# Kernel tuning notes

Measured on AMD Instinct MI355X. Metric: run time of the kernel, lower is better.

## Reference

```python
import jax, jax.numpy as jnp
import numpy as np

N_NODES = 50000


def mean_aggregate(x, src, dst):
    # gather source features, scatter-sum to destinations, divide by in-degree
    msgs = x[src]                                             # [E, D]
    summed = jax.ops.segment_sum(msgs, dst, num_segments=N_NODES)  # [N, D]
    deg = jax.ops.segment_sum(jnp.ones_like(dst, dtype=x.dtype), dst,
                              num_segments=N_NODES)           # [N]
    return summed / jnp.clip(deg, 1.0)[:, None]


def sage_conv(x, src, dst, Wl, Wr, b):
    # PyG SAGEConv (aggr='mean'): lin_l(agg) + lin_r(x); bias only on lin_l
    agg = mean_aggregate(x, src, dst)
    return agg @ Wl + b + x @ Wr


def setup_inputs() -> dict:
    key = jax.random.key(0)
    ks = jax.random.split(key, 8)
    x = jax.random.normal(ks[0], (N_NODES, 64), dtype=jnp.float32)
    edge_index = jax.random.randint(ks[1], (2, 800000), 0, N_NODES, dtype=jnp.int32)
    W1l = jax.random.normal(ks[2], (64, 128), dtype=jnp.float32) * (1.0 / np.sqrt(64))
    W1r = jax.random.normal(ks[3], (64, 128), dtype=jnp.float32) * (1.0 / np.sqrt(64))
    b1 = jnp.zeros((128,), dtype=jnp.float32)
    W2l = jax.random.normal(ks[4], (128, 40), dtype=jnp.float32) * (1.0 / np.sqrt(128))
    W2r = jax.random.normal(ks[5], (128, 40), dtype=jnp.float32) * (1.0 / np.sqrt(128))
    b2 = jnp.zeros((40,), dtype=jnp.float32)
    return {"x": x, "edge_index": edge_index, "W1l": W1l, "W1r": W1r, "b1": b1,
            "W2l": W2l, "W2r": W2r, "b2": b2}


def reference(x, edge_index, W1l, W1r, b1, W2l, W2r, b2):
    src, dst = edge_index[0], edge_index[1]
    h = sage_conv(x, src, dst, W1l, W1r, b1)
    h = jax.nn.relu(h)
    # dropout p=0.5 is identity in eval mode (self.training=False)
    h = sage_conv(h, src, dst, W2l, W2r, b2)
    return h, jax.nn.log_softmax(h, axis=1)
```

## Files before the change

### kernel.cpp

```cpp
#include <hip/hip_runtime.h>
#include <hip/hip_bf16.h>
#include <math.h>

#define N_NODES 50000
#define N_EDGES 800000
#define D0 64
#define D1 128
#define D2 40
#define SLOTS 64

typedef short s16x8 __attribute__((ext_vector_type(8)));
typedef float f32x4 __attribute__((ext_vector_type(4)));

static __device__ __forceinline__ unsigned short f2bf(float v) {
    __hip_bfloat16 hb = __float2bfloat16(v);
    return *(unsigned short*)&hb;
}

__global__ __launch_bounds__(256) void prep_scatter_kernel(
        const float* __restrict__ x, const int* __restrict__ src, const int* __restrict__ dst,
        const float* __restrict__ W1l, const float* __restrict__ W1r,
        const float* __restrict__ W2l, const float* __restrict__ W2r,
        unsigned short* __restrict__ xh, int* __restrict__ deg, int* __restrict__ csr,
        unsigned short* __restrict__ wpk1, unsigned short* __restrict__ wpk2,
        int E, int nScat, int nCast) {
    int b = blockIdx.x, t = threadIdx.x;
    if (b < nScat) {
        int e0 = b * 2048;
#pragma unroll
        for (int i = t; i < 2048; i += 256) {
            int e = e0 + i;
            if (e < E) {
                int d = dst[e];
                int s = src[e];
                int slot = atomicAdd(&deg[d], 1);
                if (slot < SLOTS) csr[((size_t)d << 6) + slot] = s;
            }
        }
    } else if (b < nScat + nCast) {
        int i = ((b - nScat) * 256 + t) * 4;
        float4 v = *(const float4*)(x + i);
        unsigned o0 = (unsigned)f2bf(v.x) | ((unsigned)f2bf(v.y) << 16);
        unsigned o1 = (unsigned)f2bf(v.z) | ((unsigned)f2bf(v.w) << 16);
        uint2 pk; pk.x = o0; pk.y = o1;
        *(uint2*)(xh + i) = pk;
    } else if (b < nScat + nCast + 8) {
        int f = (b - nScat - nCast) * 4 + (t >> 6);
        int lane = t & 63;
        int nt = f & 7;
        int col = nt * 16 + (lane & 15);
        int kbase = (f >> 3) * 32 + (lane >> 4) * 8;
        unsigned short* o = wpk1 + ((size_t)f * 64 + lane) * 8;
#pragma unroll
        for (int j = 0; j < 8; ++j) {
            int k = kbase + j;
            float w = (k < 64) ? W1r[k * 128 + col] : W1l[(k - 64) * 128 + col];
            o[j] = f2bf(w);
        }
    } else {
        int f = (b - nScat - nCast - 8) * 4 + (t >> 6);
        if (f < 20) {
            int lane = t & 63;
            int nt = f % 5;
            int col = nt * 16 + (lane & 15);
            int kbase = (f / 5) * 32 + (lane >> 4) * 8;
            unsigned short* o = wpk2 + ((size_t)f * 64 + lane) * 8;
#pragma unroll
            for (int j = 0; j < 8; ++j) {
                int k = kbase + j;
                float w = (col < 40) ? W2l[k * 40 + col] : W2r[k * 40 + (col - 40)];
                o[j] = f2bf(w);
            }
        }
    }
}


__global__ void agg1_kernel(const unsigned short* __restrict__ xh,
                            const int* __restrict__ rowcnt,
                            const int* __restrict__ csr, unsigned short* __restrict__ aggh, int N) {
    int wid = (blockIdx.x * blockDim.x + threadIdx.x) >> 6;
    int lane = threadIdx.x & 63;
    if (wid >= N) return;
    int beg = wid << 6;
    int deg = rowcnt[wid];
    int l = lane & 7, g = lane >> 3;
    float acc[8];
#pragma unroll
    for (int k = 0; k < 8; ++k) acc[k] = 0.f;
    int jmax = (deg + 7) >> 3;
    int full = jmax - 1;
    int j = 0;
    for (; j + 2 <= full; j += 2) {
        int s0 = csr[beg + j * 8 + g];
        int s1 = csr[beg + (j + 1) * 8 + g];
        uint4 v0 = *(const uint4*)(xh + (size_t)s0 * D0 + l * 8);
        uint4 v1 = *(const uint4*)(xh + (size_t)s1 * D0 + l * 8);
        acc[0] += __uint_as_float(v0.x << 16);          acc[1] += __uint_as_float(v0.x & 0xffff0000u);
        acc[2] += __uint_as_float(v0.y << 16);          acc[3] += __uint_as_float(v0.y & 0xffff0000u);
        acc[4] += __uint_as_float(v0.z << 16);          acc[5] += __uint_as_float(v0.z & 0xffff0000u);
        acc[6] += __uint_as_float(v0.w << 16);          acc[7] += __uint_as_float(v0.w & 0xffff0000u);
        acc[0] += __uint_as_float(v1.x << 16);          acc[1] += __uint_as_float(v1.x & 0xffff0000u);
        acc[2] += __uint_as_float(v1.y << 16);          acc[3] += __uint_as_float(v1.y & 0xffff0000u);
        acc[4] += __uint_as_float(v1.z << 16);          acc[5] += __uint_as_float(v1.z & 0xffff0000u);
        acc[6] += __uint_as_float(v1.w << 16);          acc[7] += __uint_as_float(v1.w & 0xffff0000u);
    }
    if (j < full) {
        int s0 = csr[beg + j * 8 + g];
        uint4 v0 = *(const uint4*)(xh + (size_t)s0 * D0 + l * 8);
        acc[0] += __uint_as_float(v0.x << 16);          acc[1] += __uint_as_float(v0.x & 0xffff0000u);
        acc[2] += __uint_as_float(v0.y << 16);          acc[3] += __uint_as_float(v0.y & 0xffff0000u);
        acc[4] += __uint_as_float(v0.z << 16);          acc[5] += __uint_as_float(v0.z & 0xffff0000u);
        acc[6] += __uint_as_float(v0.w << 16);          acc[7] += __uint_as_float(v0.w & 0xffff0000u);
    }
    if (jmax > 0) {
        int slot = full * 8 + g;
        int e = beg + ((slot < deg) ? slot : (deg - 1));
        int s0 = csr[e];
        float w = (slot < deg) ? 1.f : 0.f;
        uint4 v0 = *(const uint4*)(xh + (size_t)s0 * D0 + l * 8);
        acc[0] = fmaf(w, __uint_as_float(v0.x << 16), acc[0]);
        acc[1] = fmaf(w, __uint_as_float(v0.x & 0xffff0000u), acc[1]);
        acc[2] = fmaf(w, __uint_as_float(v0.y << 16), acc[2]);
        acc[3] = fmaf(w, __uint_as_float(v0.y & 0xffff0000u), acc[3]);
        acc[4] = fmaf(w, __uint_as_float(v0.z << 16), acc[4]);
        acc[5] = fmaf(w, __uint_as_float(v0.z & 0xffff0000u), acc[5]);
        acc[6] = fmaf(w, __uint_as_float(v0.w << 16), acc[6]);
        acc[7] = fmaf(w, __uint_as_float(v0.w & 0xffff0000u), acc[7]);
    }
#pragma unroll
    for (int off = 8; off <= 32; off <<= 1) {
#pragma unroll
        for (int k = 0; k < 8; ++k) acc[k] += __shfl_xor(acc[k], off);
    }
    float inv = 1.f / (float)max(deg, 1);
    if (g == 0) {
        unsigned o0 = (unsigned)f2bf(acc[0] * inv) | ((unsigned)f2bf(acc[1] * inv) << 16);
        unsigned o1 = (unsigned)f2bf(acc[2] * inv) | ((unsigned)f2bf(acc[3] * inv) << 16);
        unsigned o2 = (unsigned)f2bf(acc[4] * inv) | ((unsigned)f2bf(acc[5] * inv) << 16);
        unsigned o3 = (unsigned)f2bf(acc[6] * inv) | ((unsigned)f2bf(acc[7] * inv) << 16);
        uint4 pk; pk.x = o0; pk.y = o1; pk.z = o2; pk.w = o3;
        *(uint4*)(aggh + (size_t)wid * D0 + l * 8) = pk;
    }
}


__global__ void agg2_kernel(const unsigned short* __restrict__ p2h, const float* __restrict__ r2,
                            const int* __restrict__ rowcnt,
                            const int* __restrict__ csr,
                            float* __restrict__ out, float* __restrict__ out2, int N) {
    int wid = (blockIdx.x * blockDim.x + threadIdx.x) >> 6;
    int lane = threadIdx.x & 63;
    if (wid >= N) return;
    int beg = wid << 6;
    int deg = rowcnt[wid];
    int g = lane / 5;
    int l = lane - g * 5;
    bool gv = g < 12;
    float a[8];
#pragma unroll
    for (int k = 0; k < 8; ++k) a[k] = 0.f;
    int jmax = (deg + 11) / 12;
    int full = jmax - 1;
    int j = 0;
    for (; j + 2 <= full; j += 2) {
        int s0 = csr[beg + j * 12 + g];
        int s1 = csr[beg + (j + 1) * 12 + g];
        uint4 v0 = *(const uint4*)(p2h + (size_t)s0 * 64 + l * 8);
        uint4 v1 = *(const uint4*)(p2h + (size_t)s1 * 64 + l * 8);
        if (gv) {
            a[0] += __uint_as_float(v0.x << 16);  a[1] += __uint_as_float(v0.x & 0xffff0000u);
            a[2] += __uint_as_float(v0.y << 16);  a[3] += __uint_as_float(v0.y & 0xffff0000u);
            a[4] += __uint_as_float(v0.z << 16);  a[5] += __uint_as_float(v0.z & 0xffff0000u);
            a[6] += __uint_as_float(v0.w << 16);  a[7] += __uint_as_float(v0.w & 0xffff0000u);
            a[0] += __uint_as_float(v1.x << 16);  a[1] += __uint_as_float(v1.x & 0xffff0000u);
            a[2] += __uint_as_float(v1.y << 16);  a[3] += __uint_as_float(v1.y & 0xffff0000u);
            a[4] += __uint_as_float(v1.z << 16);  a[5] += __uint_as_float(v1.z & 0xffff0000u);
            a[6] += __uint_as_float(v1.w << 16);  a[7] += __uint_as_float(v1.w & 0xffff0000u);
        }
    }
    if (j < full) {
        int s0 = csr[beg + j * 12 + g];
        uint4 v0 = *(const uint4*)(p2h + (size_t)s0 * 64 + l * 8);
        if (gv) {
            a[0] += __uint_as_float(v0.x << 16);  a[1] += __uint_as_float(v0.x & 0xffff0000u);
            a[2] += __uint_as_float(v0.y << 16);  a[3] += __uint_as_float(v0.y & 0xffff0000u);
            a[4] += __uint_as_float(v0.z << 16);  a[5] += __uint_as_float(v0.z & 0xffff0000u);
            a[6] += __uint_as_float(v0.w << 16);  a[7] += __uint_as_float(v0.w & 0xffff0000u);
        }
    }
    if (jmax > 0) {
        int slot = full * 12 + g;
        int e = beg + ((slot < deg) ? slot : (deg - 1));
        int s0 = csr[e];
        float w = (gv && slot < deg) ? 1.f : 0.f;
        uint4 v0 = *(const uint4*)(p2h + (size_t)s0 * 64 + l * 8);
        a[0] = fmaf(w, __uint_as_float(v0.x << 16), a[0]);
        a[1] = fmaf(w, __uint_as_float(v0.x & 0xffff0000u), a[1]);
        a[2] = fmaf(w, __uint_as_float(v0.y << 16), a[2]);
        a[3] = fmaf(w, __uint_as_float(v0.y & 0xffff0000u), a[3]);
        a[4] = fmaf(w, __uint_as_float(v0.z << 16), a[4]);
        a[5] = fmaf(w, __uint_as_float(v0.z & 0xffff0000u), a[5]);
        a[6] = fmaf(w, __uint_as_float(v0.w << 16), a[6]);
        a[7] = fmaf(w, __uint_as_float(v0.w & 0xffff0000u), a[7]);
    }
    {
        float b0;
#pragma unroll
        for (int k = 0; k < 8; ++k) { b0 = __shfl(a[k], lane + 30); if (g < 6) a[k] += b0; }
#pragma unroll
        for (int k = 0; k < 8; ++k) { b0 = __shfl(a[k], lane + 15); if (g < 3) a[k] += b0; }
#pragma unroll
        for (int k = 0; k < 8; ++k) {
            float b1 = __shfl(a[k], lane + 5);
            float b2 = __shfl(a[k], lane + 10);
            if (g == 0) a[k] += b1 + b2;
        }
    }
    float inv = 1.f / (float)max(deg, 1);
    bool wr = (lane < 5);
    float h2[8];
    if (wr) {
        float4 ra = *(const float4*)(r2 + (size_t)wid * D2 + lane * 8);
        float4 rb = *(const float4*)(r2 + (size_t)wid * D2 + lane * 8 + 4);
        h2[0] = ra.x + a[0] * inv; h2[1] = ra.y + a[1] * inv;
        h2[2] = ra.z + a[2] * inv; h2[3] = ra.w + a[3] * inv;
        h2[4] = rb.x + a[4] * inv; h2[5] = rb.y + a[5] * inv;
        h2[6] = rb.z + a[6] * inv; h2[7] = rb.w + a[7] * inv;
        float4 oa; oa.x = h2[0]; oa.y = h2[1]; oa.z = h2[2]; oa.w = h2[3];
        float4 ob; ob.x = h2[4]; ob.y = h2[5]; ob.z = h2[6]; ob.w = h2[7];
        *(float4*)(out + (size_t)wid * D2 + lane * 8) = oa;
        *(float4*)(out + (size_t)wid * D2 + lane * 8 + 4) = ob;
    }
    float m = -INFINITY;
    if (wr) {
#pragma unroll
        for (int k = 0; k < 8; ++k) m = fmaxf(m, h2[k]);
    }
#pragma unroll
    for (int off = 1; off < 64; off <<= 1) m = fmaxf(m, __shfl_xor(m, off));
    float s = 0.f;
    if (wr) {
#pragma unroll
        for (int k = 0; k < 8; ++k) s += expf(h2[k] - m);
    }
#pragma unroll
    for (int off = 1; off < 64; off <<= 1) s += __shfl_xor(s, off);
    if (wr) {
        float lg = m + logf(s);
        float4 oa; oa.x = h2[0] - lg; oa.y = h2[1] - lg; oa.z = h2[2] - lg; oa.w = h2[3] - lg;
        float4 ob; ob.x = h2[4] - lg; ob.y = h2[5] - lg; ob.z = h2[6] - lg; ob.w = h2[7] - lg;
        *(float4*)(out2 + (size_t)wid * D2 + lane * 8) = oa;
        *(float4*)(out2 + (size_t)wid * D2 + lane * 8 + 4) = ob;
    }
}

__global__ __launch_bounds__(256) void gemm_fused(
        const unsigned short* __restrict__ xh, const unsigned short* __restrict__ aggh,
        const unsigned short* __restrict__ Wpk1, const unsigned short* __restrict__ Wpk2,
        const float* __restrict__ b1, const float* __restrict__ b2,
        unsigned short* __restrict__ p2h, float* __restrict__ r2, int N) {
    __shared__ __align__(16) unsigned short As[64 * 136];
    int t = threadIdx.x;
    int r0 = blockIdx.x * 64;
    for (int i = t; i < 1024; i += 256) {
        int r = i >> 4, c = i & 15;
        int gr = r0 + r; gr = (gr < N) ? gr : (N - 1);
        uint4 v = (c < 8) ? ((const uint4*)(xh + (size_t)gr * 64))[c]
                          : ((const uint4*)(aggh + (size_t)gr * 64))[c - 8];
        *(uint4*)(As + r * 136 + c * 8) = v;
    }
    __syncthreads();
    int w = t >> 6, lane = t & 63;
    int l15 = lane & 15, q = lane >> 4;
    f32x4 zero = {0.f, 0.f, 0.f, 0.f};
    const unsigned short* abase = As + (w * 16 + l15) * 136 + q * 8;

    f32x4 acc[8];
#pragma unroll
    for (int nt = 0; nt < 8; ++nt) acc[nt] = zero;
#pragma unroll
    for (int ks = 0; ks < 4; ++ks) {
        s16x8 a0 = *(const s16x8*)(abase + ks * 32);
        s16x8 b[8];
#pragma unroll
        for (int nt = 0; nt < 8; ++nt)
            b[nt] = *(const s16x8*)(Wpk1 + ((size_t)(ks * 8 + nt) * 64 + lane) * 8);
#pragma unroll
        for (int nt = 0; nt < 8; ++nt)
            acc[nt] = __builtin_amdgcn_mfma_f32_16x16x32_bf16(a0, b[nt], acc[nt], 0, 0, 0);
    }
    int rloc = w * 16 + q * 4;
#pragma unroll
    for (int nt = 0; nt < 8; ++nt) {
        int col = nt * 16 + l15;
        float bias = b1[col];
#pragma unroll
        for (int reg = 0; reg < 4; ++reg)
            As[(rloc + reg) * 136 + col] = f2bf(fmaxf(acc[nt][reg] + bias, 0.f));
    }
    f32x4 acc2[5];
#pragma unroll
    for (int nt = 0; nt < 5; ++nt) acc2[nt] = zero;
#pragma unroll
    for (int ks = 0; ks < 4; ++ks) {
        s16x8 a0 = *(const s16x8*)(abase + ks * 32);
        s16x8 b[5];
#pragma unroll
        for (int nt = 0; nt < 5; ++nt)
            b[nt] = *(const s16x8*)(Wpk2 + ((size_t)(ks * 5 + nt) * 64 + lane) * 8);
#pragma unroll
        for (int nt = 0; nt < 5; ++nt)
            acc2[nt] = __builtin_amdgcn_mfma_f32_16x16x32_bf16(a0, b[nt], acc2[nt], 0, 0, 0);
    }
    int rbase = r0 + w * 16 + q * 4;
#pragma unroll
    for (int nt = 0; nt < 5; ++nt) {
        int col = nt * 16 + l15;
        bool isp = col < 40;
        int oc = isp ? col : (col - 40);
        float bias = isp ? 0.f : b2[oc];
#pragma unroll
        for (int reg = 0; reg < 4; ++reg) {
            int row = rbase + reg;
            if (row < N) {
                float v = acc2[nt][reg] + bias;
                if (isp) p2h[(size_t)row * 64 + oc] = f2bf(v);
                else     r2[(size_t)row * D2 + oc] = v;
            }
        }
    }
}


extern "C" void kernel_launch(void* const* d_in, const int* in_sizes, int n_in,
                              void* d_out, int out_size, void* d_ws, size_t ws_size,
                              hipStream_t stream) {
    const float* x   = (const float*)d_in[0];
    const int*   ei  = (const int*)d_in[1];
    const float* W1l = (const float*)d_in[2];
    const float* W1r = (const float*)d_in[3];
    const float* b1  = (const float*)d_in[4];
    const float* W2l = (const float*)d_in[5];
    const float* W2r = (const float*)d_in[6];
    const float* b2  = (const float*)d_in[7];
    float* out = (float*)d_out;

    const int N = N_NODES;
    const int E = in_sizes[1] / 2;
    const int* src = ei;
    const int* dst = ei + E;

    char* p = (char*)d_ws;
    auto alloc = [&](size_t bytes) -> void* {
        void* r = (void*)p;
        p += (bytes + 255) & ~(size_t)255;
        return r;
    };
    const int nScat = (E + 2047) / 2048;
    const int nCast = (N * D0) / 1024;

    int*      deg  = (int*)alloc((size_t)N * 4);
    int*      csr  = (int*)alloc((size_t)N * SLOTS * 4);
    unsigned short* xh    = (unsigned short*)alloc((size_t)N * D0 * 2);
    unsigned short* aggh  = (unsigned short*)alloc((size_t)N * D0 * 2);
    unsigned short* wpk1  = (unsigned short*)alloc((size_t)32 * 64 * 8 * 2);
    unsigned short* wpk2  = (unsigned short*)alloc((size_t)20 * 64 * 8 * 2);
    unsigned short* p2h   = (unsigned short*)alloc((size_t)N * 64 * 2);
    float* r2buf = (float*)alloc((size_t)N * D2 * 4);

    hipMemsetAsync(deg, 0, (size_t)N * sizeof(int), stream);
    prep_scatter_kernel<<<nScat + nCast + 8 + 5, 256, 0, stream>>>(
        x, src, dst, W1l, W1r, W2l, W2r, xh, deg, csr, wpk1, wpk2, E, nScat, nCast);

    agg1_kernel<<<(N * 64 + 255) / 256, 256, 0, stream>>>(xh, deg, csr, aggh, N);
    gemm_fused<<<(N + 63) / 64, 256, 0, stream>>>(xh, aggh, wpk1, wpk2, b1, b2,
                                                  p2h, r2buf, N);

    agg2_kernel<<<(N * 64 + 255) / 256, 256, 0, stream>>>(p2h, r2buf, deg, csr,
                                                          out, out + (size_t)N * D2, N);
}
```

Baseline: 192.9 us.

## Replace per-node CSR with destination buckets and shared-memory atomic aggregation

Edges are binned into 512 buckets of 98 destination nodes using block-local histograms and one global atomic per bucket, storing packed (local dst, src) words. Both aggregation kernels now process one bucket per block, accumulating features with LDS float atomics and computing degrees locally, replacing the padded 64-slot per-node CSR and the per-node global atomics. This reduces global atomic traffic and CSR memory, but it trades in lower block-level parallelism, heavy shared-memory atomics, and a serial per-thread log-softmax epilogue with strided stores. Buckets overflowing 2048 edges would silently drop edges.

```diff
diff --git a/kernel.cpp b/kernel.cpp
--- a/kernel.cpp
+++ b/kernel.cpp
@@ -7,7 +7,12 @@
 #define D0 64
 #define D1 128
 #define D2 40
-#define SLOTS 64
+
+#define NB  512
+#define NPB 98
+#define CAP 2048
+#define PAD1 68
+#define PAD2 41
 
 typedef short s16x8 __attribute__((ext_vector_type(8)));
 typedef float f32x4 __attribute__((ext_vector_type(4)));
@@ -21,20 +26,38 @@
         const float* __restrict__ x, const int* __restrict__ src, const int* __restrict__ dst,
         const float* __restrict__ W1l, const float* __restrict__ W1r,
         const float* __restrict__ W2l, const float* __restrict__ W2r,
-        unsigned short* __restrict__ xh, int* __restrict__ deg, int* __restrict__ csr,
+        unsigned short* __restrict__ xh, int* __restrict__ gcur, unsigned* __restrict__ ebuf,
         unsigned short* __restrict__ wpk1, unsigned short* __restrict__ wpk2,
         int E, int nScat, int nCast) {
     int b = blockIdx.x, t = threadIdx.x;
     if (b < nScat) {
-        int e0 = b * 2048;
-#pragma unroll
-        for (int i = t; i < 2048; i += 256) {
-            int e = e0 + i;
-            if (e < E) {
-                int d = dst[e];
-                int s = src[e];
-                int slot = atomicAdd(&deg[d], 1);
-                if (slot < SLOTS) csr[((size_t)d << 6) + slot] = s;
+        __shared__ int h[NB];
+        __shared__ int base[NB];
+        int e0 = b * 4096;
+        h[t] = 0; h[t + 256] = 0;
+        __syncthreads();
+        int dloc[16];
+#pragma unroll
+        for (int u = 0; u < 16; ++u) {
+            int e = e0 + u * 256 + t;
+            dloc[u] = (e < E) ? dst[e] : -1;
+            if (dloc[u] >= 0) atomicAdd(&h[(unsigned)dloc[u] / NPB], 1);
+        }
+        __syncthreads();
+        for (int u = t; u < NB; u += 256)
+            if (h[u] > 0) base[u] = u * CAP + atomicAdd(&gcur[u], h[u]);
+        __syncthreads();
+        h[t] = 0; h[t + 256] = 0;
+        __syncthreads();
+#pragma unroll
+        for (int u = 0; u < 16; ++u) {
+            int e = e0 + u * 256 + t;
+            if (dloc[u] >= 0) {
+                unsigned d = (unsigned)dloc[u];
+                unsigned bk = d / NPB;
+                unsigned ld = d - bk * NPB;
+                int k = atomicAdd(&h[bk], 1);
+                ebuf[base[bk] + k] = (ld << 17) | (unsigned)src[e];
             }
         }
     } else if (b < nScat + nCast) {
@@ -75,183 +98,124 @@
     }
 }
 
-
-__global__ void agg1_kernel(const unsigned short* __restrict__ xh,
-                            const int* __restrict__ rowcnt,
-                            const int* __restrict__ csr, unsigned short* __restrict__ aggh, int N) {
-    int wid = (blockIdx.x * blockDim.x + threadIdx.x) >> 6;
-    int lane = threadIdx.x & 63;
-    if (wid >= N) return;
-    int beg = wid << 6;
-    int deg = rowcnt[wid];
-    int l = lane & 7, g = lane >> 3;
-    float acc[8];
-#pragma unroll
-    for (int k = 0; k < 8; ++k) acc[k] = 0.f;
-    int jmax = (deg + 7) >> 3;
-    int full = jmax - 1;
-    int j = 0;
-    for (; j + 2 <= full; j += 2) {
-        int s0 = csr[beg + j * 8 + g];
-        int s1 = csr[beg + (j + 1) * 8 + g];
-        uint4 v0 = *(const uint4*)(xh + (size_t)s0 * D0 + l * 8);
-        uint4 v1 = *(const uint4*)(xh + (size_t)s1 * D0 + l * 8);
-        acc[0] += __uint_as_float(v0.x << 16);          acc[1] += __uint_as_float(v0.x & 0xffff0000u);
-        acc[2] += __uint_as_float(v0.y << 16);          acc[3] += __uint_as_float(v0.y & 0xffff0000u);
-        acc[4] += __uint_as_float(v0.z << 16);          acc[5] += __uint_as_float(v0.z & 0xffff0000u);
-        acc[6] += __uint_as_float(v0.w << 16);          acc[7] += __uint_as_float(v0.w & 0xffff0000u);
-        acc[0] += __uint_as_float(v1.x << 16);          acc[1] += __uint_as_float(v1.x & 0xffff0000u);
-        acc[2] += __uint_as_float(v1.y << 16);          acc[3] += __uint_as_float(v1.y & 0xffff0000u);
-        acc[4] += __uint_as_float(v1.z << 16);          acc[5] += __uint_as_float(v1.z & 0xffff0000u);
-        acc[6] += __uint_as_float(v1.w << 16);          acc[7] += __uint_as_float(v1.w & 0xffff0000u);
-    }
-    if (j < full) {
-        int s0 = csr[beg + j * 8 + g];
-        uint4 v0 = *(const uint4*)(xh + (size_t)s0 * D0 + l * 8);
-        acc[0] += __uint_as_float(v0.x << 16);          acc[1] += __uint_as_float(v0.x & 0xffff0000u);
-        acc[2] += __uint_as_float(v0.y << 16);          acc[3] += __uint_as_float(v0.y & 0xffff0000u);
-        acc[4] += __uint_as_float(v0.z << 16);          acc[5] += __uint_as_float(v0.z & 0xffff0000u);
-        acc[6] += __uint_as_float(v0.w << 16);          acc[7] += __uint_as_float(v0.w & 0xffff0000u);
-    }
-    if (jmax > 0) {
-        int slot = full * 8 + g;
-        int e = beg + ((slot < deg) ? slot : (deg - 1));
-        int s0 = csr[e];
-        float w = (slot < deg) ? 1.f : 0.f;
-        uint4 v0 = *(const uint4*)(xh + (size_t)s0 * D0 + l * 8);
-        acc[0] = fmaf(w, __uint_as_float(v0.x << 16), acc[0]);
-        acc[1] = fmaf(w, __uint_as_float(v0.x & 0xffff0000u), acc[1]);
-        acc[2] = fmaf(w, __uint_as_float(v0.y << 16), acc[2]);
-        acc[3] = fmaf(w, __uint_as_float(v0.y & 0xffff0000u), acc[3]);
-        acc[4] = fmaf(w, __uint_as_float(v0.z << 16), acc[4]);
-        acc[5] = fmaf(w, __uint_as_float(v0.z & 0xffff0000u), acc[5]);
-        acc[6] = fmaf(w, __uint_as_float(v0.w << 16), acc[6]);
-        acc[7] = fmaf(w, __uint_as_float(v0.w & 0xffff0000u), acc[7]);
-    }
-#pragma unroll
-    for (int off = 8; off <= 32; off <<= 1) {
-#pragma unroll
-        for (int k = 0; k < 8; ++k) acc[k] += __shfl_xor(acc[k], off);
-    }
-    float inv = 1.f / (float)max(deg, 1);
-    if (g == 0) {
-        unsigned o0 = (unsigned)f2bf(acc[0] * inv) | ((unsigned)f2bf(acc[1] * inv) << 16);
-        unsigned o1 = (unsigned)f2bf(acc[2] * inv) | ((unsigned)f2bf(acc[3] * inv) << 16);
-        unsigned o2 = (unsigned)f2bf(acc[4] * inv) | ((unsigned)f2bf(acc[5] * inv) << 16);
-        unsigned o3 = (unsigned)f2bf(acc[6] * inv) | ((unsigned)f2bf(acc[7] * inv) << 16);
+__global__ __launch_bounds__(256) void agg1_bucket(
+        const unsigned short* __restrict__ xh, const unsigned* __restrict__ ebuf,
+        const int* __restrict__ gcur, unsigned short* __restrict__ aggh, int N) {
+    __shared__ float acc[NPB][PAD1];
+    __shared__ int degL[NPB];
+    int b = blockIdx.x, t = threadIdx.x;
+    for (int i = t; i < NPB * PAD1; i += 256) ((float*)acc)[i] = 0.f;
+    if (t < NPB) degL[t] = 0;
+    __syncthreads();
+    int ne = gcur[b]; ne = (ne < CAP) ? ne : CAP;
+    const unsigned* eb = ebuf + (size_t)b * CAP;
+    int l = t & 7;
+    int g = t >> 3;
+    for (int i0 = 0; i0 < ne; i0 += 128) {
+        unsigned pk[4]; uint4 v[4]; bool val[4];
+#pragma unroll
+        for (int u = 0; u < 4; ++u) {
+            int e = i0 + u * 32 + g;
+            val[u] = e < ne;
+            pk[u] = eb[val[u] ? e : 0];
+            int sid = val[u] ? (int)(pk[u] & 0x1FFFFu) : 0;
+            v[u] = *(const uint4*)(xh + (size_t)sid * D0 + l * 8);
+        }
+#pragma unroll
+        for (int u = 0; u < 4; ++u) {
+            if (val[u]) {
+                int ld = (int)(pk[u] >> 17);
+                float* a = &acc[ld][l * 8];
+                atomicAdd(&a[0], __uint_as_float(v[u].x << 16));
+                atomicAdd(&a[1], __uint_as_float(v[u].x & 0xffff0000u));
+                atomicAdd(&a[2], __uint_as_float(v[u].y << 16));
+                atomicAdd(&a[3], __uint_as_float(v[u].y & 0xffff0000u));
+                atomicAdd(&a[4], __uint_as_float(v[u].z << 16));
+                atomicAdd(&a[5], __uint_as_float(v[u].z & 0xffff0000u));
+                atomicAdd(&a[6], __uint_as_float(v[u].w << 16));
+                atomicAdd(&a[7], __uint_as_float(v[u].w & 0xffff0000u));
+                if (l == 0) atomicAdd(&degL[ld], 1);
+            }
+        }
+    }
+    __syncthreads();
+    for (int i = t; i < NPB * 8; i += 256) {
+        int n = i >> 3, l8 = (i & 7) * 8;
+        int node = b * NPB + n;
+        if (node >= N) continue;
+        float inv = 1.f / (float)max(degL[n], 1);
+        const float* a = &acc[n][l8];
+        unsigned o0 = (unsigned)f2bf(a[0] * inv) | ((unsigned)f2bf(a[1] * inv) << 16);
+        unsigned o1 = (unsigned)f2bf(a[2] * inv) | ((unsigned)f2bf(a[3] * inv) << 16);
+        unsigned o2 = (unsigned)f2bf(a[4] * inv) | ((unsigned)f2bf(a[5] * inv) << 16);
+        unsigned o3 = (unsigned)f2bf(a[6] * inv) | ((unsigned)f2bf(a[7] * inv) << 16);
         uint4 pk; pk.x = o0; pk.y = o1; pk.z = o2; pk.w = o3;
-        *(uint4*)(aggh + (size_t)wid * D0 + l * 8) = pk;
-    }
-}
-
-
-__global__ void agg2_kernel(const unsigned short* __restrict__ p2h, const float* __restrict__ r2,
-                            const int* __restrict__ rowcnt,
-                            const int* __restrict__ csr,
-                            float* __restrict__ out, float* __restrict__ out2, int N) {
-    int wid = (blockIdx.x * blockDim.x + threadIdx.x) >> 6;
-    int lane = threadIdx.x & 63;
-    if (wid >= N) return;
-    int beg = wid << 6;
-    int deg = rowcnt[wid];
-    int g = lane / 5;
-    int l = lane - g * 5;
-    bool gv = g < 12;
-    float a[8];
-#pragma unroll
-    for (int k = 0; k < 8; ++k) a[k] = 0.f;
-    int jmax = (deg + 11) / 12;
-    int full = jmax - 1;
-    int j = 0;
-    for (; j + 2 <= full; j += 2) {
-        int s0 = csr[beg + j * 12 + g];
-        int s1 = csr[beg + (j + 1) * 12 + g];
-        uint4 v0 = *(const uint4*)(p2h + (size_t)s0 * 64 + l * 8);
-        uint4 v1 = *(const uint4*)(p2h + (size_t)s1 * 64 + l * 8);
-        if (gv) {
-            a[0] += __uint_as_float(v0.x << 16);  a[1] += __uint_as_float(v0.x & 0xffff0000u);
-            a[2] += __uint_as_float(v0.y << 16);  a[3] += __uint_as_float(v0.y & 0xffff0000u);
-            a[4] += __uint_as_float(v0.z << 16);  a[5] += __uint_as_float(v0.z & 0xffff0000u);
-            a[6] += __uint_as_float(v0.w << 16);  a[7] += __uint_as_float(v0.w & 0xffff0000u);
-            a[0] += __uint_as_float(v1.x << 16);  a[1] += __uint_as_float(v1.x & 0xffff0000u);
-            a[2] += __uint_as_float(v1.y << 16);  a[3] += __uint_as_float(v1.y & 0xffff0000u);
-            a[4] += __uint_as_float(v1.z << 16);  a[5] += __uint_as_float(v1.z & 0xffff0000u);
-            a[6] += __uint_as_float(v1.w << 16);  a[7] += __uint_as_float(v1.w & 0xffff0000u);
-        }
-    }
-    if (j < full) {
-        int s0 = csr[beg + j * 12 + g];
-        uint4 v0 = *(const uint4*)(p2h + (size_t)s0 * 64 + l * 8);
-        if (gv) {
-            a[0] += __uint_as_float(v0.x << 16);  a[1] += __uint_as_float(v0.x & 0xffff0000u);
-            a[2] += __uint_as_float(v0.y << 16);  a[3] += __uint_as_float(v0.y & 0xffff0000u);
-            a[4] += __uint_as_float(v0.z << 16);  a[5] += __uint_as_float(v0.z & 0xffff0000u);
-            a[6] += __uint_as_float(v0.w << 16);  a[7] += __uint_as_float(v0.w & 0xffff0000u);
-        }
-    }
-    if (jmax > 0) {
-        int slot = full * 12 + g;
-        int e = beg + ((slot < deg) ? slot : (deg - 1));
-        int s0 = csr[e];
-        float w = (gv && slot < deg) ? 1.f : 0.f;
-        uint4 v0 = *(const uint4*)(p2h + (size_t)s0 * 64 + l * 8);
-        a[0] = fmaf(w, __uint_as_float(v0.x << 16), a[0]);
-        a[1] = fmaf(w, __uint_as_float(v0.x & 0xffff0000u), a[1]);
-        a[2] = fmaf(w, __uint_as_float(v0.y << 16), a[2]);
-        a[3] = fmaf(w, __uint_as_float(v0.y & 0xffff0000u), a[3]);
-        a[4] = fmaf(w, __uint_as_float(v0.z << 16), a[4]);
-        a[5] = fmaf(w, __uint_as_float(v0.z & 0xffff0000u), a[5]);
-        a[6] = fmaf(w, __uint_as_float(v0.w << 16), a[6]);
-        a[7] = fmaf(w, __uint_as_float(v0.w & 0xffff0000u), a[7]);
-    }
-    {
-        float b0;
-#pragma unroll
-        for (int k = 0; k < 8; ++k) { b0 = __shfl(a[k], lane + 30); if (g < 6) a[k] += b0; }
-#pragma unroll
-        for (int k = 0; k < 8; ++k) { b0 = __shfl(a[k], lane + 15); if (g < 3) a[k] += b0; }
-#pragma unroll
-        for (int k = 0; k < 8; ++k) {
-            float b1 = __shfl(a[k], lane + 5);
-            float b2 = __shfl(a[k], lane + 10);
-            if (g == 0) a[k] += b1 + b2;
-        }
-    }
-    float inv = 1.f / (float)max(deg, 1);
-    bool wr = (lane < 5);
-    float h2[8];
-    if (wr) {
-        float4 ra = *(const float4*)(r2 + (size_t)wid * D2 + lane * 8);
-        float4 rb = *(const float4*)(r2 + (size_t)wid * D2 + lane * 8 + 4);
-        h2[0] = ra.x + a[0] * inv; h2[1] = ra.y + a[1] * inv;
-        h2[2] = ra.z + a[2] * inv; h2[3] = ra.w + a[3] * inv;
-        h2[4] = rb.x + a[4] * inv; h2[5] = rb.y + a[5] * inv;
-        h2[6] = rb.z + a[6] * inv; h2[7] = rb.w + a[7] * inv;
-        float4 oa; oa.x = h2[0]; oa.y = h2[1]; oa.z = h2[2]; oa.w = h2[3];
-        float4 ob; ob.x = h2[4]; ob.y = h2[5]; ob.z = h2[6]; ob.w = h2[7];
-        *(float4*)(out + (size_t)wid * D2 + lane * 8) = oa;
-        *(float4*)(out + (size_t)wid * D2 + lane * 8 + 4) = ob;
-    }
-    float m = -INFINITY;
-    if (wr) {
-#pragma unroll
-        for (int k = 0; k < 8; ++k) m = fmaxf(m, h2[k]);
-    }
-#pragma unroll
-    for (int off = 1; off < 64; off <<= 1) m = fmaxf(m, __shfl_xor(m, off));
-    float s = 0.f;
-    if (wr) {
-#pragma unroll
-        for (int k = 0; k < 8; ++k) s += expf(h2[k] - m);
-    }
-#pragma unroll
-    for (int off = 1; off < 64; off <<= 1) s += __shfl_xor(s, off);
-    if (wr) {
-        float lg = m + logf(s);
-        float4 oa; oa.x = h2[0] - lg; oa.y = h2[1] - lg; oa.z = h2[2] - lg; oa.w = h2[3] - lg;
-        float4 ob; ob.x = h2[4] - lg; ob.y = h2[5] - lg; ob.z = h2[6] - lg; ob.w = h2[7] - lg;
-        *(float4*)(out2 + (size_t)wid * D2 + lane * 8) = oa;
-        *(float4*)(out2 + (size_t)wid * D2 + lane * 8 + 4) = ob;
+        *(uint4*)(aggh + (size_t)node * D0 + l8) = pk;
+    }
+}
+
+__global__ __launch_bounds__(256) void agg2_bucket(
+        const unsigned short* __restrict__ p2h, const float* __restrict__ r2,
+        const unsigned* __restrict__ ebuf, const int* __restrict__ gcur,
+        float* __restrict__ out, float* __restrict__ out2, int N) {
+    __shared__ float acc[NPB][PAD2];
+    __shared__ int degL[NPB];
+    int b = blockIdx.x, t = threadIdx.x;
+    for (int i = t; i < NPB * PAD2; i += 256) ((float*)acc)[i] = 0.f;
+    if (t < NPB) degL[t] = 0;
+    __syncthreads();
+    int ne = gcur[b]; ne = (ne < CAP) ? ne : CAP;
+    const unsigned* eb = ebuf + (size_t)b * CAP;
+    int g = t / 5;
+    int l = t - g * 5;
+    bool gv = g < 51;
+    for (int i0 = 0; i0 < ne; i0 += 204) {
+        unsigned pk[4]; uint4 v[4]; bool val[4];
+#pragma unroll
+        for (int u = 0; u < 4; ++u) {
+            int e = i0 + u * 51 + g;
+            val[u] = gv && (e < ne);
+            pk[u] = eb[val[u] ? e : 0];
+            int sid = val[u] ? (int)(pk[u] & 0x1FFFFu) : 0;
+            v[u] = *(const uint4*)(p2h + (size_t)sid * 64 + l * 8);
+        }
+#pragma unroll
+        for (int u = 0; u < 4; ++u) {
+            if (val[u]) {
+                int ld = (int)(pk[u] >> 17);
+                float* a = &acc[ld][l * 8];
+                atomicAdd(&a[0], __uint_as_float(v[u].x << 16));
+                atomicAdd(&a[1], __uint_as_float(v[u].x & 0xffff0000u));
+                atomicAdd(&a[2], __uint_as_float(v[u].y << 16));
+                atomicAdd(&a[3], __uint_as_float(v[u].y & 0xffff0000u));
+                atomicAdd(&a[4], __uint_as_float(v[u].z << 16));
+                atomicAdd(&a[5], __uint_as_float(v[u].z & 0xffff0000u));
+                atomicAdd(&a[6], __uint_as_float(v[u].w << 16));
+                atomicAdd(&a[7], __uint_as_float(v[u].w & 0xffff0000u));
+                if (l == 0) atomicAdd(&degL[ld], 1);
+            }
+        }
+    }
+    __syncthreads();
+    if (t < NPB) {
+        int node = b * NPB + t;
+        if (node < N) {
+            float inv = 1.f / (float)max(degL[t], 1);
+            const float* rr = r2 + (size_t)node * D2;
+            float* ha = acc[t];
+            float m = -INFINITY;
+            for (int d = 0; d < D2; ++d) {
+                float h = rr[d] + ha[d] * inv;
+                ha[d] = h;
+                out[(size_t)node * D2 + d] = h;
+                m = fmaxf(m, h);
+            }
+            float s = 0.f;
+            for (int d = 0; d < D2; ++d) s += expf(ha[d] - m);
+            float lg = m + logf(s);
+            for (int d = 0; d < D2; ++d)
+                out2[(size_t)node * D2 + d] = ha[d] - lg;
+        }
     }
 }
 
@@ -357,11 +321,11 @@
         p += (bytes + 255) & ~(size_t)255;
         return r;
     };
-    const int nScat = (E + 2047) / 2048;
+    const int nScat = (E + 4095) / 4096;
     const int nCast = (N * D0) / 1024;
 
-    int*      deg  = (int*)alloc((size_t)N * 4);
-    int*      csr  = (int*)alloc((size_t)N * SLOTS * 4);
+    unsigned* ebuf = (unsigned*)alloc((size_t)NB * CAP * 4);
+    int*      gcur = (int*)alloc(NB * 4);
     unsigned short* xh    = (unsigned short*)alloc((size_t)N * D0 * 2);
     unsigned short* aggh  = (unsigned short*)alloc((size_t)N * D0 * 2);
     unsigned short* wpk1  = (unsigned short*)alloc((size_t)32 * 64 * 8 * 2);
@@ -369,14 +333,14 @@
     unsigned short* p2h   = (unsigned short*)alloc((size_t)N * 64 * 2);
     float* r2buf = (float*)alloc((size_t)N * D2 * 4);
 
-    hipMemsetAsync(deg, 0, (size_t)N * sizeof(int), stream);
+    hipMemsetAsync(gcur, 0, NB * sizeof(int), stream);
     prep_scatter_kernel<<<nScat + nCast + 8 + 5, 256, 0, stream>>>(
-        x, src, dst, W1l, W1r, W2l, W2r, xh, deg, csr, wpk1, wpk2, E, nScat, nCast);
-
-    agg1_kernel<<<(N * 64 + 255) / 256, 256, 0, stream>>>(xh, deg, csr, aggh, N);
+        x, src, dst, W1l, W1r, W2l, W2r, xh, gcur, ebuf, wpk1, wpk2, E, nScat, nCast);
+
+    agg1_bucket<<<NB, 256, 0, stream>>>(xh, ebuf, gcur, aggh, N);
     gemm_fused<<<(N + 63) / 64, 256, 0, stream>>>(xh, aggh, wpk1, wpk2, b1, b2,
                                                   p2h, r2buf, N);
 
-    agg2_kernel<<<(N * 64 + 255) / 256, 256, 0, stream>>>(p2h, r2buf, deg, csr,
-                                                          out, out + (size_t)N * D2, N);
-}
+    agg2_bucket<<<NB, 256, 0, stream>>>(p2h, r2buf, ebuf, gcur,
+                                        out, out + (size_t)N * D2, N);
+}
```

Result: slower. 555.5 us (+188.0%).

## Replace per-node slot CSR with bucketed two-pass edge sort and fused agg1

Applied to the files above, without the earlier changes.

Edge scattering changes from per-node global atomics into fixed 64-slot rows to a two-level bucket sort. Each block builds a shared-memory histogram of 49-node buckets, reserves space with one global atomic per bucket, and writes packed (local dst, src) words. A new fused kernel then builds a compact per-bucket CSR in LDS, emits rowstart/rowcnt for layer 2, and runs layer-1 aggregation directly from the LDS CSR. The aim is fewer contended global atomics and a smaller, denser CSR. The cost is a fixed per-bucket capacity of 1024 edges, which silently drops edges if a bucket overflows, and only 1024 blocks for the aggregation.

```diff
diff --git a/kernel.cpp b/kernel.cpp
--- a/kernel.cpp
+++ b/kernel.cpp
@@ -3,11 +3,13 @@
 #include <math.h>
 
 #define N_NODES 50000
-#define N_EDGES 800000
 #define D0 64
 #define D1 128
 #define D2 40
-#define SLOTS 64
+
+#define NB  1024
+#define NPB 49
+#define CAP 1024
 
 typedef short s16x8 __attribute__((ext_vector_type(8)));
 typedef float f32x4 __attribute__((ext_vector_type(4)));
@@ -21,20 +23,38 @@
         const float* __restrict__ x, const int* __restrict__ src, const int* __restrict__ dst,
         const float* __restrict__ W1l, const float* __restrict__ W1r,
         const float* __restrict__ W2l, const float* __restrict__ W2r,
-        unsigned short* __restrict__ xh, int* __restrict__ deg, int* __restrict__ csr,
+        unsigned short* __restrict__ xh, int* __restrict__ gcur, unsigned* __restrict__ ebuf,
         unsigned short* __restrict__ wpk1, unsigned short* __restrict__ wpk2,
         int E, int nScat, int nCast) {
     int b = blockIdx.x, t = threadIdx.x;
     if (b < nScat) {
-        int e0 = b * 2048;
-#pragma unroll
-        for (int i = t; i < 2048; i += 256) {
-            int e = e0 + i;
-            if (e < E) {
-                int d = dst[e];
-                int s = src[e];
-                int slot = atomicAdd(&deg[d], 1);
-                if (slot < SLOTS) csr[((size_t)d << 6) + slot] = s;
+        __shared__ int h[NB];
+        __shared__ int base[NB];
+        int e0 = b * 4096;
+        h[t] = 0; h[t + 256] = 0; h[t + 512] = 0; h[t + 768] = 0;
+        __syncthreads();
+        int dloc[16];
+#pragma unroll
+        for (int u = 0; u < 16; ++u) {
+            int e = e0 + u * 256 + t;
+            dloc[u] = (e < E) ? dst[e] : -1;
+            if (dloc[u] >= 0) atomicAdd(&h[(unsigned)dloc[u] / NPB], 1);
+        }
+        __syncthreads();
+        for (int u = t; u < NB; u += 256)
+            if (h[u] > 0) base[u] = u * CAP + atomicAdd(&gcur[u], h[u]);
+        __syncthreads();
+        h[t] = 0; h[t + 256] = 0; h[t + 512] = 0; h[t + 768] = 0;
+        __syncthreads();
+#pragma unroll
+        for (int u = 0; u < 16; ++u) {
+            int e = e0 + u * 256 + t;
+            if (dloc[u] >= 0) {
+                unsigned d = (unsigned)dloc[u];
+                unsigned bk = d / NPB;
+                unsigned ld = d - bk * NPB;
+                int k = atomicAdd(&h[bk], 1);
+                ebuf[base[bk] + k] = (ld << 17) | (unsigned)src[e];
             }
         }
     } else if (b < nScat + nCast) {
@@ -75,84 +95,139 @@
     }
 }
 
-
-__global__ void agg1_kernel(const unsigned short* __restrict__ xh,
-                            const int* __restrict__ rowcnt,
-                            const int* __restrict__ csr, unsigned short* __restrict__ aggh, int N) {
-    int wid = (blockIdx.x * blockDim.x + threadIdx.x) >> 6;
-    int lane = threadIdx.x & 63;
-    if (wid >= N) return;
-    int beg = wid << 6;
-    int deg = rowcnt[wid];
+__global__ __launch_bounds__(256) void fillagg1_kernel(
+        const unsigned short* __restrict__ xh, const unsigned* __restrict__ ebuf,
+        const int* __restrict__ gcur,
+        int* __restrict__ rowstart, int* __restrict__ rowcnt, int* __restrict__ csr,
+        unsigned short* __restrict__ aggh, int N) {
+    __shared__ int csr_l[CAP];
+    __shared__ int cnt[64];
+    __shared__ int sd[64];
+    __shared__ int rs[64];
+    __shared__ int pos[64];
+    int b = blockIdx.x, t = threadIdx.x;
+    int s0 = b * CAP;
+    int ne = gcur[b]; ne = (ne < CAP) ? ne : CAP;
+    unsigned ev[4];
+#pragma unroll
+    for (int u = 0; u < 4; ++u) {
+        int i = t + u * 256;
+        ev[u] = (i < ne) ? ebuf[s0 + i] : 0xFFFFFFFFu;
+    }
+    if (t < 64) cnt[t] = 0;
+    __syncthreads();
+#pragma unroll
+    for (int u = 0; u < 4; ++u)
+        if (ev[u] != 0xFFFFFFFFu) atomicAdd(&cnt[ev[u] >> 17], 1);
+    __syncthreads();
+    if (t < 64) sd[t] = cnt[t];
+    __syncthreads();
+    for (int off = 1; off < 64; off <<= 1) {
+        int u = (t >= off && t < 64) ? sd[t - off] : 0;
+        __syncthreads();
+        if (t < 64) sd[t] += u;
+        __syncthreads();
+    }
+    if (t < 64) {
+        int ex = sd[t] - cnt[t];
+        rs[t] = ex;
+        pos[t] = ex;
+    }
+    __syncthreads();
+#pragma unroll
+    for (int u = 0; u < 4; ++u) {
+        if (ev[u] != 0xFFFFFFFFu) {
+            int ld = (int)(ev[u] >> 17);
+            int p = atomicAdd(&pos[ld], 1);
+            csr_l[p] = (int)(ev[u] & 0x1FFFFu);
+        }
+    }
+    if (t < NPB) {
+        int node = b * NPB + t;
+        if (node < N) {
+            rowstart[node] = s0 + rs[t];
+            rowcnt[node] = cnt[t];
+        }
+    }
+    __syncthreads();
+    for (int i = t; i < ne; i += 256) csr[s0 + i] = csr_l[i];
+
+    int w = t >> 6, lane = t & 63;
     int l = lane & 7, g = lane >> 3;
-    float acc[8];
-#pragma unroll
-    for (int k = 0; k < 8; ++k) acc[k] = 0.f;
-    int jmax = (deg + 7) >> 3;
-    int full = jmax - 1;
-    int j = 0;
-    for (; j + 2 <= full; j += 2) {
-        int s0 = csr[beg + j * 8 + g];
-        int s1 = csr[beg + (j + 1) * 8 + g];
-        uint4 v0 = *(const uint4*)(xh + (size_t)s0 * D0 + l * 8);
-        uint4 v1 = *(const uint4*)(xh + (size_t)s1 * D0 + l * 8);
-        acc[0] += __uint_as_float(v0.x << 16);          acc[1] += __uint_as_float(v0.x & 0xffff0000u);
-        acc[2] += __uint_as_float(v0.y << 16);          acc[3] += __uint_as_float(v0.y & 0xffff0000u);
-        acc[4] += __uint_as_float(v0.z << 16);          acc[5] += __uint_as_float(v0.z & 0xffff0000u);
-        acc[6] += __uint_as_float(v0.w << 16);          acc[7] += __uint_as_float(v0.w & 0xffff0000u);
-        acc[0] += __uint_as_float(v1.x << 16);          acc[1] += __uint_as_float(v1.x & 0xffff0000u);
-        acc[2] += __uint_as_float(v1.y << 16);          acc[3] += __uint_as_float(v1.y & 0xffff0000u);
-        acc[4] += __uint_as_float(v1.z << 16);          acc[5] += __uint_as_float(v1.z & 0xffff0000u);
-        acc[6] += __uint_as_float(v1.w << 16);          acc[7] += __uint_as_float(v1.w & 0xffff0000u);
-    }
-    if (j < full) {
-        int s0 = csr[beg + j * 8 + g];
-        uint4 v0 = *(const uint4*)(xh + (size_t)s0 * D0 + l * 8);
-        acc[0] += __uint_as_float(v0.x << 16);          acc[1] += __uint_as_float(v0.x & 0xffff0000u);
-        acc[2] += __uint_as_float(v0.y << 16);          acc[3] += __uint_as_float(v0.y & 0xffff0000u);
-        acc[4] += __uint_as_float(v0.z << 16);          acc[5] += __uint_as_float(v0.z & 0xffff0000u);
-        acc[6] += __uint_as_float(v0.w << 16);          acc[7] += __uint_as_float(v0.w & 0xffff0000u);
-    }
-    if (jmax > 0) {
-        int slot = full * 8 + g;
-        int e = beg + ((slot < deg) ? slot : (deg - 1));
-        int s0 = csr[e];
-        float w = (slot < deg) ? 1.f : 0.f;
-        uint4 v0 = *(const uint4*)(xh + (size_t)s0 * D0 + l * 8);
-        acc[0] = fmaf(w, __uint_as_float(v0.x << 16), acc[0]);
-        acc[1] = fmaf(w, __uint_as_float(v0.x & 0xffff0000u), acc[1]);
-        acc[2] = fmaf(w, __uint_as_float(v0.y << 16), acc[2]);
-        acc[3] = fmaf(w, __uint_as_float(v0.y & 0xffff0000u), acc[3]);
-        acc[4] = fmaf(w, __uint_as_float(v0.z << 16), acc[4]);
-        acc[5] = fmaf(w, __uint_as_float(v0.z & 0xffff0000u), acc[5]);
-        acc[6] = fmaf(w, __uint_as_float(v0.w << 16), acc[6]);
-        acc[7] = fmaf(w, __uint_as_float(v0.w & 0xffff0000u), acc[7]);
-    }
-#pragma unroll
-    for (int off = 8; off <= 32; off <<= 1) {
-#pragma unroll
-        for (int k = 0; k < 8; ++k) acc[k] += __shfl_xor(acc[k], off);
-    }
-    float inv = 1.f / (float)max(deg, 1);
-    if (g == 0) {
-        unsigned o0 = (unsigned)f2bf(acc[0] * inv) | ((unsigned)f2bf(acc[1] * inv) << 16);
-        unsigned o1 = (unsigned)f2bf(acc[2] * inv) | ((unsigned)f2bf(acc[3] * inv) << 16);
-        unsigned o2 = (unsigned)f2bf(acc[4] * inv) | ((unsigned)f2bf(acc[5] * inv) << 16);
-        unsigned o3 = (unsigned)f2bf(acc[6] * inv) | ((unsigned)f2bf(acc[7] * inv) << 16);
-        uint4 pk; pk.x = o0; pk.y = o1; pk.z = o2; pk.w = o3;
-        *(uint4*)(aggh + (size_t)wid * D0 + l * 8) = pk;
+    for (int n = w; n < NPB; n += 4) {
+        int node = b * NPB + n;
+        if (node >= N) break;
+        int beg = rs[n];
+        int deg = cnt[n];
+        float acc[8];
+#pragma unroll
+        for (int k = 0; k < 8; ++k) acc[k] = 0.f;
+        int jmax = (deg + 7) >> 3;
+        int full = jmax - 1;
+        int j = 0;
+        for (; j + 2 <= full; j += 2) {
+            int s0e = csr_l[beg + j * 8 + g];
+            int s1e = csr_l[beg + (j + 1) * 8 + g];
+            uint4 v0 = *(const uint4*)(xh + (size_t)s0e * D0 + l * 8);
+            uint4 v1 = *(const uint4*)(xh + (size_t)s1e * D0 + l * 8);
+            acc[0] += __uint_as_float(v0.x << 16);  acc[1] += __uint_as_float(v0.x & 0xffff0000u);
+            acc[2] += __uint_as_float(v0.y << 16);  acc[3] += __uint_as_float(v0.y & 0xffff0000u);
+            acc[4] += __uint_as_float(v0.z << 16);  acc[5] += __uint_as_float(v0.z & 0xffff0000u);
+            acc[6] += __uint_as_float(v0.w << 16);  acc[7] += __uint_as_float(v0.w & 0xffff0000u);
+            acc[0] += __uint_as_float(v1.x << 16);  acc[1] += __uint_as_float(v1.x & 0xffff0000u);
+            acc[2] += __uint_as_float(v1.y << 16);  acc[3] += __uint_as_float(v1.y & 0xffff0000u);
+            acc[4] += __uint_as_float(v1.z << 16);  acc[5] += __uint_as_float(v1.z & 0xffff0000u);
+            acc[6] += __uint_as_float(v1.w << 16);  acc[7] += __uint_as_float(v1.w & 0xffff0000u);
+        }
+        if (j < full) {
+            int s0e = csr_l[beg + j * 8 + g];
+            uint4 v0 = *(const uint4*)(xh + (size_t)s0e * D0 + l * 8);
+            acc[0] += __uint_as_float(v0.x << 16);  acc[1] += __uint_as_float(v0.x & 0xffff0000u);
+            acc[2] += __uint_as_float(v0.y << 16);  acc[3] += __uint_as_float(v0.y & 0xffff0000u);
+            acc[4] += __uint_as_float(v0.z << 16);  acc[5] += __uint_as_float(v0.z & 0xffff0000u);
+            acc[6] += __uint_as_float(v0.w << 16);  acc[7] += __uint_as_float(v0.w & 0xffff0000u);
+        }
+        if (jmax > 0) {
+            int slot = full * 8 + g;
+            int e = beg + ((slot < deg) ? slot : (deg - 1));
+            int s0e = csr_l[e];
+            float wgt = (slot < deg) ? 1.f : 0.f;
+            uint4 v0 = *(const uint4*)(xh + (size_t)s0e * D0 + l * 8);
+            acc[0] = fmaf(wgt, __uint_as_float(v0.x << 16), acc[0]);
+            acc[1] = fmaf(wgt, __uint_as_float(v0.x & 0xffff0000u), acc[1]);
+            acc[2] = fmaf(wgt, __uint_as_float(v0.y << 16), acc[2]);
+            acc[3] = fmaf(wgt, __uint_as_float(v0.y & 0xffff0000u), acc[3]);
+            acc[4] = fmaf(wgt, __uint_as_float(v0.z << 16), acc[4]);
+            acc[5] = fmaf(wgt, __uint_as_float(v0.z & 0xffff0000u), acc[5]);
+            acc[6] = fmaf(wgt, __uint_as_float(v0.w << 16), acc[6]);
+            acc[7] = fmaf(wgt, __uint_as_float(v0.w & 0xffff0000u), acc[7]);
+        }
+#pragma unroll
+        for (int off = 8; off <= 32; off <<= 1) {
+#pragma unroll
+            for (int k = 0; k < 8; ++k) acc[k] += __shfl_xor(acc[k], off);
+        }
+        float inv = 1.f / (float)max(deg, 1);
+        if (g == 0) {
+            unsigned o0 = (unsigned)f2bf(acc[0] * inv) | ((unsigned)f2bf(acc[1] * inv) << 16);
+            unsigned o1 = (unsigned)f2bf(acc[2] * inv) | ((unsigned)f2bf(acc[3] * inv) << 16);
+            unsigned o2 = (unsigned)f2bf(acc[4] * inv) | ((unsigned)f2bf(acc[5] * inv) << 16);
+            unsigned o3 = (unsigned)f2bf(acc[6] * inv) | ((unsigned)f2bf(acc[7] * inv) << 16);
+            uint4 pk; pk.x = o0; pk.y = o1; pk.z = o2; pk.w = o3;
+            *(uint4*)(aggh + (size_t)node * D0 + l * 8) = pk;
+        }
     }
 }
 
 
 __global__ void agg2_kernel(const unsigned short* __restrict__ p2h, const float* __restrict__ r2,
-                            const int* __restrict__ rowcnt,
+                            const int* __restrict__ rowstart, const int* __restrict__ rowcnt,
                             const int* __restrict__ csr,
                             float* __restrict__ out, float* __restrict__ out2, int N) {
     int wid = (blockIdx.x * blockDim.x + threadIdx.x) >> 6;
     int lane = threadIdx.x & 63;
     if (wid >= N) return;
-    int beg = wid << 6;
+    int beg = rowstart[wid];
     int deg = rowcnt[wid];
     int g = lane / 5;
     int l = lane - g * 5;
@@ -212,9 +287,9 @@
         for (int k = 0; k < 8; ++k) { b0 = __shfl(a[k], lane + 15); if (g < 3) a[k] += b0; }
 #pragma unroll
         for (int k = 0; k < 8; ++k) {
-            float b1 = __shfl(a[k], lane + 5);
-            float b2 = __shfl(a[k], lane + 10);
-            if (g == 0) a[k] += b1 + b2;
+            float c1 = __shfl(a[k], lane + 5);
+            float c2 = __shfl(a[k], lane + 10);
+            if (g == 0) a[k] += c1 + c2;
         }
     }
     float inv = 1.f / (float)max(deg, 1);
@@ -357,11 +432,14 @@
         p += (bytes + 255) & ~(size_t)255;
         return r;
     };
-    const int nScat = (E + 2047) / 2048;
+    const int nScat = (E + 4095) / 4096;
     const int nCast = (N * D0) / 1024;
 
-    int*      deg  = (int*)alloc((size_t)N * 4);
-    int*      csr  = (int*)alloc((size_t)N * SLOTS * 4);
+    unsigned* ebuf     = (unsigned*)alloc((size_t)NB * CAP * 4);
+    int*      csr      = (int*)alloc((size_t)NB * CAP * 4);
+    int*      gcur     = (int*)alloc(NB * 4);
+    int*      rowstart = (int*)alloc((size_t)N * 4);
+    int*      rowcnt   = (int*)alloc((size_t)N * 4);
     unsigned short* xh    = (unsigned short*)alloc((size_t)N * D0 * 2);
     unsigned short* aggh  = (unsigned short*)alloc((size_t)N * D0 * 2);
     unsigned short* wpk1  = (unsigned short*)alloc((size_t)32 * 64 * 8 * 2);
@@ -369,14 +447,15 @@
     unsigned short* p2h   = (unsigned short*)alloc((size_t)N * 64 * 2);
     float* r2buf = (float*)alloc((size_t)N * D2 * 4);
 
-    hipMemsetAsync(deg, 0, (size_t)N * sizeof(int), stream);
+    hipMemsetAsync(gcur, 0, NB * sizeof(int), stream);
     prep_scatter_kernel<<<nScat + nCast + 8 + 5, 256, 0, stream>>>(
-        x, src, dst, W1l, W1r, W2l, W2r, xh, deg, csr, wpk1, wpk2, E, nScat, nCast);
-
-    agg1_kernel<<<(N * 64 + 255) / 256, 256, 0, stream>>>(xh, deg, csr, aggh, N);
+        x, src, dst, W1l, W1r, W2l, W2r, xh, gcur, ebuf, wpk1, wpk2, E, nScat, nCast);
+
+    fillagg1_kernel<<<NB, 256, 0, stream>>>(xh, ebuf, gcur, rowstart, rowcnt, csr, aggh, N);
+
     gemm_fused<<<(N + 63) / 64, 256, 0, stream>>>(xh, aggh, wpk1, wpk2, b1, b2,
                                                   p2h, r2buf, N);
 
-    agg2_kernel<<<(N * 64 + 255) / 256, 256, 0, stream>>>(p2h, r2buf, deg, csr,
+    agg2_kernel<<<(N * 64 + 255) / 256, 256, 0, stream>>>(p2h, r2buf, rowstart, rowcnt, csr,
                                                           out, out + (size_t)N * D2, N);
 }
```

After: 169.6 us. 12.1% less time.
